# Kernel optimization log

Hardware: AMD Instinct MI355X
Metric: run time of the kernel (lower is better)

The kernel has to match this reference:

```python
import jax, jax.numpy as jnp
import numpy as np

HIDDEN = 1024
INTER = 2048
NUM_EXPERTS = 8
TOP_K = 2
GROUP_SIZE = 128
TOKENS = 4096


def _dequant_int4(packed, scale, group_size):
    # packed: [E, N, K//2] ints in [0,256) holding two uint4 nibbles (low | high<<4)
    # scale:  [E, N, K//group_size] float32
    E, N, Kh = packed.shape
    K = 2 * Kh
    low = packed & 0xF
    high = (packed >> 4) & 0xF
    # interleave: even K positions = low nibble, odd = high nibble
    q = jnp.stack([low, high], axis=-1).reshape(E, N, K) - 8  # int4 values in [-8,7]
    q = q.astype(jnp.float32).reshape(E, N, K // group_size, group_size)
    w = q * scale[..., None]
    return w.reshape(E, N, K)


def setup_inputs() -> dict:
    key = jax.random.key(0)
    k1, k2, k3, k4, k5, k6 = jax.random.split(key, 6)
    x = jax.random.normal(k1, (TOKENS, HIDDEN), dtype=jnp.float32)
    router_w = jax.random.normal(k2, (NUM_EXPERTS, HIDDEN), dtype=jnp.float32) * 0.02
    w1 = jax.random.randint(k3, (NUM_EXPERTS, 2 * INTER, HIDDEN // 2), 0, 256, dtype=jnp.int32)
    w1_scale = jax.random.uniform(k4, (NUM_EXPERTS, 2 * INTER, HIDDEN // GROUP_SIZE), dtype=jnp.float32) * 0.05
    w2 = jax.random.randint(k5, (NUM_EXPERTS, HIDDEN, INTER // 2), 0, 256, dtype=jnp.int32)
    w2_scale = jax.random.uniform(k6, (NUM_EXPERTS, HIDDEN, INTER // GROUP_SIZE), dtype=jnp.float32) * 0.05
    return {"x": x, "router_w": router_w, "w1": w1, "w1_scale": w1_scale, "w2": w2, "w2_scale": w2_scale}


def reference(x, router_w, w1, w1_scale, w2, w2_scale):
    # Router: topk then softmax over the top-k logits
    scores = x @ router_w.T                                 # [T, E]
    top_w, top_i = jax.lax.top_k(scores, TOP_K)             # [T, K]
    top_w = jax.nn.softmax(top_w, axis=-1).astype(jnp.float32)

    # Dequantize int4 grouped weights once
    w1_deq = _dequant_int4(w1, w1_scale, GROUP_SIZE)        # [E, 2I, H]
    w2_deq = _dequant_int4(w2, w2_scale, GROUP_SIZE)        # [E, H, I]

    out = jnp.zeros_like(x)
    for e in range(NUM_EXPERTS):
        # per-token routing weight for expert e (0 if not routed)
        ge = jnp.sum(top_w * (top_i == e), axis=-1)         # [T]
        h = x @ w1_deq[e].T                                  # [T, 2I]
        gate, up = h[:, :INTER], h[:, INTER:]
        a = jax.nn.silu(gate) * up                           # SwiGLU
        y = a @ w2_deq[e].T                                  # [T, H]
        out = out + ge[:, None] * y
    return out
```

## Files before the change

### kernel.cpp

```cpp
#include <hip/hip_runtime.h>
#include <hip/hip_bf16.h>

#define HIDDEN 1024
#define INTER 2048
#define NE 8
#define GS 128
#define TOKENS 4096
#define MAXROWS 9216
#define MAXTILES 72

typedef __bf16 bf16x8 __attribute__((ext_vector_type(8)));
typedef float f32x4 __attribute__((ext_vector_type(4)));

#define OFF_TOPKI 0u
#define OFF_TOPKW 32768u
#define OFF_CTRL  65536u
#define OFF_TOK   66048u
#define OFF_SLOT  102912u
#define OFF_TILE  135680u
#define OFF_XG    139776u
#define OFF_A     19014144u
#define OFF_W1D   56762880u
#define OFF_W2D   123871744u

__device__ __forceinline__ unsigned short f2bf(float f) {
  union { float f; unsigned int u; } v; v.f = f;
  unsigned int r = (v.u + 0x7FFFu + ((v.u >> 16) & 1u)) >> 16;
  return (unsigned short)r;
}
__device__ __forceinline__ float bf2f(unsigned int u) {
  union { unsigned int u; float f; } v; v.u = u << 16;
  return v.f;
}
__device__ __forceinline__ unsigned int pack2(unsigned short lo, unsigned short hi) {
  return (unsigned int)lo | ((unsigned int)hi << 16);
}

typedef const __attribute__((address_space(1))) unsigned int GAS;
typedef __attribute__((address_space(3))) unsigned int LAS;
__device__ __forceinline__ void gload16(const unsigned short* g, unsigned short* l) {
  __builtin_amdgcn_global_load_lds((GAS*)g, (LAS*)l, 16, 0, 0);
}


__global__ __launch_bounds__(256) void k_prep(const float* __restrict__ x,
    const float* __restrict__ rw, int* __restrict__ topki, float* __restrict__ topkw,
    const int* __restrict__ w1, const float* __restrict__ w1s,
    unsigned short* __restrict__ w1d,
    const int* __restrict__ w2, const float* __restrict__ w2s,
    unsigned short* __restrict__ w2d) {
  int bid = blockIdx.x, tid = threadIdx.x;
  if (bid >= 17408) {
    int gid = (bid - 17408) * 256 + tid;
    int i4 = gid * 4;
    int r = i4 >> 10;
    int i = i4 & 1023;
    float s = w2s[r * 16 + (i >> 6)];
    int4 p = *reinterpret_cast<const int4*>(w2 + (size_t)i4);
    int pv[4] = { p.x, p.y, p.z, p.w };
    uint4 o; unsigned int ov[4];
#pragma unroll
    for (int j = 0; j < 4; j++) {
      float lo = (float)((pv[j] & 15) - 8) * s;
      float hi = (float)(((pv[j] >> 4) & 15) - 8) * s;
      ov[j] = pack2(f2bf(lo), f2bf(hi));
    }
    o.x = ov[0]; o.y = ov[1]; o.z = ov[2]; o.w = ov[3];
    *reinterpret_cast<uint4*>(w2d + ((size_t)r << 11) + 2 * i) = o;
    return;
  }
  if (bid >= 1024) {
    int gid = (bid - 1024) * 256 + tid;
    int i4 = gid * 4;
    int r = i4 >> 9;
    int i = i4 & 511;
    float s = w1s[r * 8 + (i >> 6)];
    int4 p = *reinterpret_cast<const int4*>(w1 + (size_t)i4);
    int pv[4] = { p.x, p.y, p.z, p.w };
    uint4 o; unsigned int ov[4];
#pragma unroll
    for (int j = 0; j < 4; j++) {
      float lo = (float)((pv[j] & 15) - 8) * s;
      float hi = (float)(((pv[j] >> 4) & 15) - 8) * s;
      ov[j] = pack2(f2bf(lo), f2bf(hi));
    }
    o.x = ov[0]; o.y = ov[1]; o.z = ov[2]; o.w = ov[3];
    *reinterpret_cast<uint4*>(w1d + ((size_t)r << 10) + 2 * i) = o;
    return;
  }
  int wave = tid >> 6, lane = tid & 63;
  int t = bid * 4 + wave;
  float acc[NE];
#pragma unroll
  for (int e = 0; e < NE; e++) acc[e] = 0.f;
  const float* xr = x + (size_t)t * HIDDEN;
  for (int i = lane; i < HIDDEN; i += 64) {
    float xv = xr[i];
#pragma unroll
    for (int e = 0; e < NE; e++) acc[e] += xv * rw[e * HIDDEN + i];
  }
#pragma unroll
  for (int e = 0; e < NE; e++) {
    float v = acc[e];
    for (int off = 32; off > 0; off >>= 1) v += __shfl_down(v, off, 64);
    acc[e] = v;
  }
  if (lane == 0) {
    int b0 = 0; float s0 = acc[0];
#pragma unroll
    for (int e = 1; e < NE; e++) if (acc[e] > s0) { s0 = acc[e]; b0 = e; }
    int b1 = -1; float s1 = -3.0e38f;
#pragma unroll
    for (int e = 0; e < NE; e++) if (e != b0 && acc[e] > s1) { s1 = acc[e]; b1 = e; }
    float w0 = 1.f / (1.f + __expf(s1 - s0));
    topki[t * 2] = b0; topki[t * 2 + 1] = b1;
    topkw[t * 2] = w0; topkw[t * 2 + 1] = 1.f - w0;
  }
}

__global__ __launch_bounds__(256) void k_route2(const int* __restrict__ topki,
    int* __restrict__ ctrl, int* __restrict__ tok, int* __restrict__ slots,
    int* __restrict__ tilemap) {
  __shared__ int h[NE], off[NE], cnt[NE];
  int tid = threadIdx.x;
  if (tid < NE) h[tid] = 0;
  __syncthreads();
  for (int i = tid; i < TOKENS * 2; i += 256) atomicAdd(&h[topki[i]], 1);
  __syncthreads();
  if (tid == 0) {
    int run = 0, t = 0;
    for (int e = 0; e < NE; e++) {
      int c = h[e];
      ctrl[e] = c; ctrl[16 + e] = run; off[e] = run;
      int pc = (c + 127) & ~127;
      for (int mt = 0; mt < (pc >> 7); mt++) tilemap[t++] = (e << 20) | (run + mt * 128);
      run += pc;
    }
    ctrl[24] = run; ctrl[25] = t;
  }
  __syncthreads();
#pragma unroll
  for (int e = 0; e < NE; e++) {
    int c = h[e], pc = (c + 127) & ~127;
    for (int i = c + tid; i < pc; i += 256) tok[off[e] + i] = -1;
  }
  if (tid < NE) cnt[tid] = off[tid];
  __syncthreads();
  for (int i = tid; i < TOKENS * 2; i += 256) {
    int e = topki[i];
    int p = atomicAdd(&cnt[e], 1);
    tok[p] = i >> 1;
    slots[i] = p;
  }
}

__global__ __launch_bounds__(256) void k_gather(const float* __restrict__ x,
    const int* __restrict__ ctrl, const int* __restrict__ tok,
    unsigned short* __restrict__ xg) {
  int s = blockIdx.x;
  if (s >= ctrl[24]) return;
  int t = tok[s];
  int c = threadIdx.x * 4;
  unsigned short* dst = xg + (size_t)s * HIDDEN + c;
  if (t < 0) {
    uint2 z; z.x = 0u; z.y = 0u;
    *reinterpret_cast<uint2*>(dst) = z;
  } else {
    float4 v = *reinterpret_cast<const float4*>(x + (size_t)t * HIDDEN + c);
    uint2 o;
    o.x = pack2(f2bf(v.x), f2bf(v.y));
    o.y = pack2(f2bf(v.z), f2bf(v.w));
    *reinterpret_cast<uint2*>(dst) = o;
  }
}

__global__ __launch_bounds__(256) void k_gemm1(
    const unsigned short* __restrict__ xg, const unsigned short* __restrict__ w1d,
    const int* __restrict__ ctrl, const int* __restrict__ tilemap,
    unsigned short* __restrict__ a_out) {
  __shared__ unsigned short sA[128 * 32];
  __shared__ unsigned short sBg[64 * 32];
  __shared__ unsigned short sBu[64 * 32];
  int bid = blockIdx.x, tid = threadIdx.x;
  int nt = bid & 31, tile = bid >> 5;
  if (tile >= ctrl[25]) return;
  int tm = tilemap[tile];
  int e = tm >> 20, row0 = tm & 0xFFFFF;
  int n0 = nt * 64;
  int wave = tid >> 6, lane = tid & 63;
  int ln = lane & 15, quad = lane >> 4;
  int wr = (wave & 1) * 64, wc = (wave >> 1) * 32;

  int srow = tid >> 2, scblk = tid & 3;
  int scol = (scblk ^ ((srow >> 1) & 3)) * 8;
  const unsigned short* gA0 = xg + (size_t)(row0 + srow) * HIDDEN + scol;
  const unsigned short* gA1 = gA0 + (size_t)64 * HIDDEN;
  const unsigned short* gBg = w1d + ((size_t)e * 4096 + n0 + srow) * HIDDEN + scol;
  const unsigned short* gBu = gBg + (size_t)INTER * HIDDEN;
  unsigned short* lA0 = sA + tid * 8;
  unsigned short* lA1 = sA + 64 * 32 + tid * 8;
  unsigned short* lBg = sBg + tid * 8;
  unsigned short* lBu = sBu + tid * 8;

  f32x4 aG[4][2] = {}, aU[4][2] = {};
  for (int k0 = 0; k0 < HIDDEN; k0 += 32) {
    __syncthreads();
    gload16(gA0 + k0, lA0);
    gload16(gA1 + k0, lA1);
    gload16(gBg + k0, lBg);
    gload16(gBu + k0, lBu);
    __syncthreads();
    bf16x8 af[4], bg[2], bu[2];
#pragma unroll
    for (int m = 0; m < 4; m++) {
      int ar = wr + m * 16 + ln;
      af[m] = *reinterpret_cast<const bf16x8*>(&sA[ar * 32 + (quad ^ ((ar >> 1) & 3)) * 8]);
    }
#pragma unroll
    for (int n = 0; n < 2; n++) {
      int br = wc + n * 16 + ln;
      int bo = br * 32 + (quad ^ ((br >> 1) & 3)) * 8;
      bg[n] = *reinterpret_cast<const bf16x8*>(&sBg[bo]);
      bu[n] = *reinterpret_cast<const bf16x8*>(&sBu[bo]);
    }
#pragma unroll
    for (int m = 0; m < 4; m++)
#pragma unroll
      for (int n = 0; n < 2; n++) {
        aG[m][n] = __builtin_amdgcn_mfma_f32_16x16x32_bf16(af[m], bg[n], aG[m][n], 0, 0, 0);
        aU[m][n] = __builtin_amdgcn_mfma_f32_16x16x32_bf16(af[m], bu[n], aU[m][n], 0, 0, 0);
      }
  }
#pragma unroll
  for (int m = 0; m < 4; m++)
#pragma unroll
    for (int n = 0; n < 2; n++) {
      int col = n0 + wc + n * 16 + ln;
#pragma unroll
      for (int r = 0; r < 4; r++) {
        float g = aG[m][n][r], u = aU[m][n][r];
        float act = (g / (1.f + __expf(-g))) * u;
        int row = row0 + wr + m * 16 + quad * 4 + r;
        a_out[(size_t)row * INTER + col] = f2bf(act);
      }
    }
}

__global__ __launch_bounds__(256) void k_gemm2(
    const unsigned short* __restrict__ a_in, const unsigned short* __restrict__ w2d,
    const int* __restrict__ ctrl, const int* __restrict__ tilemap,
    unsigned short* __restrict__ y) {
  __shared__ unsigned short sA[128 * 32];
  __shared__ unsigned short sB[128 * 32];
  int bid = blockIdx.x, tid = threadIdx.x;
  int nt = bid & 7, tile = bid >> 3;
  if (tile >= ctrl[25]) return;
  int tm = tilemap[tile];
  int e = tm >> 20, row0 = tm & 0xFFFFF;
  int n0 = nt * 128;
  int wave = tid >> 6, lane = tid & 63;
  int ln = lane & 15, quad = lane >> 4;
  int wr = (wave & 1) * 64, wc = (wave >> 1) * 64;

  int srow = tid >> 2, scblk = tid & 3;
  int scol = (scblk ^ ((srow >> 1) & 3)) * 8;
  const unsigned short* gA0 = a_in + (size_t)(row0 + srow) * INTER + scol;
  const unsigned short* gA1 = gA0 + (size_t)64 * INTER;
  const unsigned short* gB0 = w2d + ((size_t)e * 1024 + n0 + srow) * INTER + scol;
  const unsigned short* gB1 = gB0 + (size_t)64 * INTER;
  unsigned short* lA0 = sA + tid * 8;
  unsigned short* lA1 = sA + 64 * 32 + tid * 8;
  unsigned short* lB0 = sB + tid * 8;
  unsigned short* lB1 = sB + 64 * 32 + tid * 8;

  f32x4 acc[4][4] = {};
  for (int k0 = 0; k0 < INTER; k0 += 32) {
    __syncthreads();
    gload16(gA0 + k0, lA0);
    gload16(gA1 + k0, lA1);
    gload16(gB0 + k0, lB0);
    gload16(gB1 + k0, lB1);
    __syncthreads();
    bf16x8 af[4], bf_[4];
#pragma unroll
    for (int m = 0; m < 4; m++) {
      int ar = wr + m * 16 + ln;
      af[m] = *reinterpret_cast<const bf16x8*>(&sA[ar * 32 + (quad ^ ((ar >> 1) & 3)) * 8]);
    }
#pragma unroll
    for (int n = 0; n < 4; n++) {
      int br = wc + n * 16 + ln;
      bf_[n] = *reinterpret_cast<const bf16x8*>(&sB[br * 32 + (quad ^ ((br >> 1) & 3)) * 8]);
    }
#pragma unroll
    for (int m = 0; m < 4; m++)
#pragma unroll
      for (int n = 0; n < 4; n++)
        acc[m][n] = __builtin_amdgcn_mfma_f32_16x16x32_bf16(af[m], bf_[n], acc[m][n], 0, 0, 0);
  }
#pragma unroll
  for (int m = 0; m < 4; m++)
#pragma unroll
    for (int n = 0; n < 4; n++) {
      int col = n0 + wc + n * 16 + ln;
#pragma unroll
      for (int r = 0; r < 4; r++) {
        int row = row0 + wr + m * 16 + quad * 4 + r;
        y[(size_t)row * HIDDEN + col] = f2bf(acc[m][n][r]);
      }
    }
}

__global__ __launch_bounds__(256) void k_combine(const unsigned short* __restrict__ y,
    const int* __restrict__ slots, const float* __restrict__ topkw,
    float* __restrict__ out) {
  int t = blockIdx.x;
  int c = threadIdx.x * 4;
  int s0 = slots[t * 2], s1 = slots[t * 2 + 1];
  float g0 = topkw[t * 2], g1 = topkw[t * 2 + 1];
  uint2 va = *reinterpret_cast<const uint2*>(y + (size_t)s0 * HIDDEN + c);
  uint2 vb = *reinterpret_cast<const uint2*>(y + (size_t)s1 * HIDDEN + c);
  float4 o;
  o.x = g0 * bf2f(va.x & 0xffffu) + g1 * bf2f(vb.x & 0xffffu);
  o.y = g0 * bf2f(va.x >> 16)     + g1 * bf2f(vb.x >> 16);
  o.z = g0 * bf2f(va.y & 0xffffu) + g1 * bf2f(vb.y & 0xffffu);
  o.w = g0 * bf2f(va.y >> 16)     + g1 * bf2f(vb.y >> 16);
  *reinterpret_cast<float4*>(out + (size_t)t * HIDDEN + c) = o;
}

extern "C" void kernel_launch(void* const* d_in, const int* in_sizes, int n_in,
                              void* d_out, int out_size, void* d_ws, size_t ws_size,
                              hipStream_t stream) {
  const float* x   = (const float*)d_in[0];
  const float* rw  = (const float*)d_in[1];
  const int*   w1  = (const int*)d_in[2];
  const float* w1s = (const float*)d_in[3];
  const int*   w2  = (const int*)d_in[4];
  const float* w2s = (const float*)d_in[5];
  float* out = (float*)d_out;
  char* ws = (char*)d_ws;

  int*   topki = (int*)(ws + OFF_TOPKI);
  float* topkw = (float*)(ws + OFF_TOPKW);
  int*   ctrl  = (int*)(ws + OFF_CTRL);
  int*   tok   = (int*)(ws + OFF_TOK);
  int*   slots = (int*)(ws + OFF_SLOT);
  int*   tilemap = (int*)(ws + OFF_TILE);
  unsigned short* xg  = (unsigned short*)(ws + OFF_XG);
  unsigned short* a   = (unsigned short*)(ws + OFF_A);
  unsigned short* w1d = (unsigned short*)(ws + OFF_W1D);
  unsigned short* w2d = (unsigned short*)(ws + OFF_W2D);

  k_prep<<<25600, 256, 0, stream>>>(x, rw, topki, topkw, w1, w1s, w1d, w2, w2s, w2d);
  k_route2<<<1, 256, 0, stream>>>(topki, ctrl, tok, slots, tilemap);
  k_gather<<<MAXROWS, 256, 0, stream>>>(x, ctrl, tok, xg);
  k_gemm1<<<32 * MAXTILES, 256, 0, stream>>>(xg, w1d, ctrl, tilemap, a);
  k_gemm2<<<8 * MAXTILES, 256, 0, stream>>>(a, w2d, ctrl, tilemap, xg );
  k_combine<<<TOKENS, 256, 0, stream>>>(xg, slots, topkw, out);
}
```

Measured before the change: 333.1 us.

## Fuse token gather into GEMM1 via index loads and split-K GEMM2

Removes the gather kernel: x is converted to bf16 in the prep kernel (plus a zero row for padding), and GEMM1 loads A rows indirectly through the token map. GEMM2 splits K in two, doubling its block count to improve CU occupancy, writing two bf16 partial outputs into the freed w1 dequant buffer, which the combine kernel sums. This costs extra partial-output traffic and an additional bf16 rounding of partials.

```diff
diff --git a/kernel.cpp b/kernel.cpp
--- a/kernel.cpp
+++ b/kernel.cpp
@@ -18,10 +18,12 @@
 #define OFF_TOK   66048u
 #define OFF_SLOT  102912u
 #define OFF_TILE  135680u
-#define OFF_XG    139776u
-#define OFF_A     19014144u
-#define OFF_W1D   56762880u
-#define OFF_W2D   123871744u
+#define OFF_XB    139776u
+#define OFF_A     8530432u
+#define OFF_W1D   46279168u
+#define OFF_W2D   113388032u
+#define OFF_Y0    OFF_W1D
+#define OFF_Y1    (OFF_W1D + 18874368u)
 
 __device__ __forceinline__ unsigned short f2bf(float f) {
   union { float f; unsigned int u; } v; v.f = f;
@@ -48,8 +50,22 @@
     const int* __restrict__ w1, const float* __restrict__ w1s,
     unsigned short* __restrict__ w1d,
     const int* __restrict__ w2, const float* __restrict__ w2s,
-    unsigned short* __restrict__ w2d) {
+    unsigned short* __restrict__ w2d, unsigned short* __restrict__ xb) {
   int bid = blockIdx.x, tid = threadIdx.x;
+  if (bid == 29696) {
+    uint2 z; z.x = 0u; z.y = 0u;
+    *reinterpret_cast<uint2*>(xb + (size_t)TOKENS * HIDDEN + tid * 4) = z;
+    return;
+  }
+  if (bid >= 25600) {
+    size_t idx = (size_t)(bid - 25600) * 1024 + tid * 4;
+    float4 v = *reinterpret_cast<const float4*>(x + idx);
+    uint2 o;
+    o.x = pack2(f2bf(v.x), f2bf(v.y));
+    o.y = pack2(f2bf(v.z), f2bf(v.w));
+    *reinterpret_cast<uint2*>(xb + idx) = o;
+    return;
+  }
   if (bid >= 17408) {
     int gid = (bid - 17408) * 256 + tid;
     int i4 = gid * 4;
@@ -154,30 +170,10 @@
   }
 }
 
-__global__ __launch_bounds__(256) void k_gather(const float* __restrict__ x,
-    const int* __restrict__ ctrl, const int* __restrict__ tok,
-    unsigned short* __restrict__ xg) {
-  int s = blockIdx.x;
-  if (s >= ctrl[24]) return;
-  int t = tok[s];
-  int c = threadIdx.x * 4;
-  unsigned short* dst = xg + (size_t)s * HIDDEN + c;
-  if (t < 0) {
-    uint2 z; z.x = 0u; z.y = 0u;
-    *reinterpret_cast<uint2*>(dst) = z;
-  } else {
-    float4 v = *reinterpret_cast<const float4*>(x + (size_t)t * HIDDEN + c);
-    uint2 o;
-    o.x = pack2(f2bf(v.x), f2bf(v.y));
-    o.y = pack2(f2bf(v.z), f2bf(v.w));
-    *reinterpret_cast<uint2*>(dst) = o;
-  }
-}
-
 __global__ __launch_bounds__(256) void k_gemm1(
-    const unsigned short* __restrict__ xg, const unsigned short* __restrict__ w1d,
+    const unsigned short* __restrict__ xb, const unsigned short* __restrict__ w1d,
     const int* __restrict__ ctrl, const int* __restrict__ tilemap,
-    unsigned short* __restrict__ a_out) {
+    const int* __restrict__ tok, unsigned short* __restrict__ a_out) {
   __shared__ unsigned short sA[128 * 32];
   __shared__ unsigned short sBg[64 * 32];
   __shared__ unsigned short sBu[64 * 32];
@@ -193,8 +189,10 @@
 
   int srow = tid >> 2, scblk = tid & 3;
   int scol = (scblk ^ ((srow >> 1) & 3)) * 8;
-  const unsigned short* gA0 = xg + (size_t)(row0 + srow) * HIDDEN + scol;
-  const unsigned short* gA1 = gA0 + (size_t)64 * HIDDEN;
+  int t0 = tok[row0 + srow];
+  int t1 = tok[row0 + 64 + srow];
+  const unsigned short* gA0 = xb + (size_t)(t0 < 0 ? TOKENS : t0) * HIDDEN + scol;
+  const unsigned short* gA1 = xb + (size_t)(t1 < 0 ? TOKENS : t1) * HIDDEN + scol;
   const unsigned short* gBg = w1d + ((size_t)e * 4096 + n0 + srow) * HIDDEN + scol;
   const unsigned short* gBu = gBg + (size_t)INTER * HIDDEN;
   unsigned short* lA0 = sA + tid * 8;
@@ -253,7 +251,7 @@
   __shared__ unsigned short sA[128 * 32];
   __shared__ unsigned short sB[128 * 32];
   int bid = blockIdx.x, tid = threadIdx.x;
-  int nt = bid & 7, tile = bid >> 3;
+  int kp = bid & 1, nt = (bid >> 1) & 7, tile = bid >> 4;
   if (tile >= ctrl[25]) return;
   int tm = tilemap[tile];
   int e = tm >> 20, row0 = tm & 0xFFFFF;
@@ -264,9 +262,10 @@
 
   int srow = tid >> 2, scblk = tid & 3;
   int scol = (scblk ^ ((srow >> 1) & 3)) * 8;
-  const unsigned short* gA0 = a_in + (size_t)(row0 + srow) * INTER + scol;
+  int kbase = kp * (INTER / 2);
+  const unsigned short* gA0 = a_in + (size_t)(row0 + srow) * INTER + kbase + scol;
   const unsigned short* gA1 = gA0 + (size_t)64 * INTER;
-  const unsigned short* gB0 = w2d + ((size_t)e * 1024 + n0 + srow) * INTER + scol;
+  const unsigned short* gB0 = w2d + ((size_t)e * 1024 + n0 + srow) * INTER + kbase + scol;
   const unsigned short* gB1 = gB0 + (size_t)64 * INTER;
   unsigned short* lA0 = sA + tid * 8;
   unsigned short* lA1 = sA + 64 * 32 + tid * 8;
@@ -274,7 +273,7 @@
   unsigned short* lB1 = sB + 64 * 32 + tid * 8;
 
   f32x4 acc[4][4] = {};
-  for (int k0 = 0; k0 < INTER; k0 += 32) {
+  for (int k0 = 0; k0 < INTER / 2; k0 += 32) {
     __syncthreads();
     gload16(gA0 + k0, lA0);
     gload16(gA1 + k0, lA1);
@@ -298,6 +297,7 @@
       for (int n = 0; n < 4; n++)
         acc[m][n] = __builtin_amdgcn_mfma_f32_16x16x32_bf16(af[m], bf_[n], acc[m][n], 0, 0, 0);
   }
+  unsigned short* yk = y + (size_t)kp * MAXROWS * HIDDEN;
 #pragma unroll
   for (int m = 0; m < 4; m++)
 #pragma unroll
@@ -306,7 +306,7 @@
 #pragma unroll
       for (int r = 0; r < 4; r++) {
         int row = row0 + wr + m * 16 + quad * 4 + r;
-        y[(size_t)row * HIDDEN + col] = f2bf(acc[m][n][r]);
+        yk[(size_t)row * HIDDEN + col] = f2bf(acc[m][n][r]);
       }
     }
 }
@@ -318,13 +318,20 @@
   int c = threadIdx.x * 4;
   int s0 = slots[t * 2], s1 = slots[t * 2 + 1];
   float g0 = topkw[t * 2], g1 = topkw[t * 2 + 1];
-  uint2 va = *reinterpret_cast<const uint2*>(y + (size_t)s0 * HIDDEN + c);
-  uint2 vb = *reinterpret_cast<const uint2*>(y + (size_t)s1 * HIDDEN + c);
+  const unsigned short* y1 = y + (size_t)MAXROWS * HIDDEN;
+  uint2 a0 = *reinterpret_cast<const uint2*>(y  + (size_t)s0 * HIDDEN + c);
+  uint2 a1 = *reinterpret_cast<const uint2*>(y1 + (size_t)s0 * HIDDEN + c);
+  uint2 b0 = *reinterpret_cast<const uint2*>(y  + (size_t)s1 * HIDDEN + c);
+  uint2 b1 = *reinterpret_cast<const uint2*>(y1 + (size_t)s1 * HIDDEN + c);
   float4 o;
-  o.x = g0 * bf2f(va.x & 0xffffu) + g1 * bf2f(vb.x & 0xffffu);
-  o.y = g0 * bf2f(va.x >> 16)     + g1 * bf2f(vb.x >> 16);
-  o.z = g0 * bf2f(va.y & 0xffffu) + g1 * bf2f(vb.y & 0xffffu);
-  o.w = g0 * bf2f(va.y >> 16)     + g1 * bf2f(vb.y >> 16);
+  o.x = g0 * (bf2f(a0.x & 0xffffu) + bf2f(a1.x & 0xffffu))
+      + g1 * (bf2f(b0.x & 0xffffu) + bf2f(b1.x & 0xffffu));
+  o.y = g0 * (bf2f(a0.x >> 16) + bf2f(a1.x >> 16))
+      + g1 * (bf2f(b0.x >> 16) + bf2f(b1.x >> 16));
+  o.z = g0 * (bf2f(a0.y & 0xffffu) + bf2f(a1.y & 0xffffu))
+      + g1 * (bf2f(b0.y & 0xffffu) + bf2f(b1.y & 0xffffu));
+  o.w = g0 * (bf2f(a0.y >> 16) + bf2f(a1.y >> 16))
+      + g1 * (bf2f(b0.y >> 16) + bf2f(b1.y >> 16));
   *reinterpret_cast<float4*>(out + (size_t)t * HIDDEN + c) = o;
 }
 
@@ -346,15 +353,15 @@
   int*   tok   = (int*)(ws + OFF_TOK);
   int*   slots = (int*)(ws + OFF_SLOT);
   int*   tilemap = (int*)(ws + OFF_TILE);
-  unsigned short* xg  = (unsigned short*)(ws + OFF_XG);
+  unsigned short* xb  = (unsigned short*)(ws + OFF_XB);
   unsigned short* a   = (unsigned short*)(ws + OFF_A);
   unsigned short* w1d = (unsigned short*)(ws + OFF_W1D);
   unsigned short* w2d = (unsigned short*)(ws + OFF_W2D);
-
-  k_prep<<<25600, 256, 0, stream>>>(x, rw, topki, topkw, w1, w1s, w1d, w2, w2s, w2d);
+  unsigned short* y   = (unsigned short*)(ws + OFF_Y0);
+
+  k_prep<<<29697, 256, 0, stream>>>(x, rw, topki, topkw, w1, w1s, w1d, w2, w2s, w2d, xb);
   k_route2<<<1, 256, 0, stream>>>(topki, ctrl, tok, slots, tilemap);
-  k_gather<<<MAXROWS, 256, 0, stream>>>(x, ctrl, tok, xg);
-  k_gemm1<<<32 * MAXTILES, 256, 0, stream>>>(xg, w1d, ctrl, tilemap, a);
-  k_gemm2<<<8 * MAXTILES, 256, 0, stream>>>(a, w2d, ctrl, tilemap, xg );
-  k_combine<<<TOKENS, 256, 0, stream>>>(xg, slots, topkw, out);
-}
+  k_gemm1<<<32 * MAXTILES, 256, 0, stream>>>(xb, w1d, ctrl, tilemap, tok, a);
+  k_gemm2<<<16 * MAXTILES, 256, 0, stream>>>(a, w2d, ctrl, tilemap, y);
+  k_combine<<<TOKENS, 256, 0, stream>>>(y, slots, topkw, out);
+}
```

Result: faster. 320.2 us (-3.9%).
